# Kernel optimization log

Measured on AMD Instinct MI355X. Metric: run time of the kernel, lower is better.

Reference implementation:

```python
import jax, jax.numpy as jnp
import numpy as np

N, C, H, W = 10, 512, 40, 40
HW = H * W
OUT_CH = 128
EPS = 1e-12

def _l2norm(x, axis):
    # matches F.normalize: v / max(||v||_2, eps)
    n = jnp.sqrt(jnp.sum(x * x, axis=axis, keepdims=True))
    return x / jnp.maximum(n, EPS)

def _conv(x, w, b, pad):
    y = jax.lax.conv_general_dilated(
        x, w, window_strides=(1, 1), padding=[(pad, pad), (pad, pad)],
        dimension_numbers=('NCHW', 'OIHW', 'NCHW'))
    return y + b[None, :, None, None]

def setup_inputs() -> dict:
    key = jax.random.key(0)
    ks = jax.random.split(key, 6)
    feats = jax.random.normal(ks[0], (N, C, H, W), jnp.float32)
    SISMs = jax.random.uniform(ks[1], (N, 1, H, W), jnp.float32)
    # ResNetBlock(HW -> 128) params (Kaiming-uniform-ish fan-in bounds)
    s1 = float(1.0 / np.sqrt(HW * 9))
    s2 = float(1.0 / np.sqrt(OUT_CH * 9))
    ss = float(1.0 / np.sqrt(HW))
    w1 = jax.random.uniform(ks[2], (OUT_CH, HW, 3, 3), jnp.float32, -s1, s1)
    b1 = jnp.zeros((OUT_CH,), jnp.float32)
    w2 = jax.random.uniform(ks[3], (OUT_CH, OUT_CH, 3, 3), jnp.float32, -s2, s2)
    b2 = jnp.zeros((OUT_CH,), jnp.float32)
    ws = jax.random.uniform(ks[4], (OUT_CH, HW, 1, 1), jnp.float32, -ss, ss)
    bs = jnp.zeros((OUT_CH,), jnp.float32)
    return dict(feats=feats, SISMs=SISMs, w1=w1, b1=b1, w2=w2, b2=b2, ws=ws, bs=bs)

def reference(feats, SISMs, w1, b1, w2, b2, ws, bs):
    # SISMs supplied at (H,W): bilinear resize w/ align_corners=True at same size is identity
    NFs = _l2norm(feats, axis=1)                                   # (N,C,H,W)
    SIVs = _l2norm(jnp.mean(NFs * SISMs, axis=(-1, -2)), axis=1)   # (N,C)
    # CFM: 1x1 conv of NFs with SIVs as filters -> (N,N,H,W)
    cm = jnp.einsum('nchw,mc->nmhw', NFs, SIVs).reshape(N, N, HW)
    cm = _l2norm(cm, axis=2)
    corr = jnp.einsum('nmk,npk->nmp', cm, cm)                      # (N,N,N)
    wv = jax.nn.softmax(jnp.sum(corr, axis=2), axis=1)             # (N,N)
    CSA = jnp.sum(cm * wv[:, :, None], axis=1)                     # (N,HW)
    mn = jnp.min(CSA, axis=1, keepdims=True)
    mx = jnp.max(CSA, axis=1, keepdims=True)
    CSA = (CSA - mn) / (mx - mn + EPS)
    CSA_maps = CSA.reshape(N, 1, H, W)
    # self-correlation features: (N, HW, H, W)
    NFf = NFs.reshape(N, C, HW)
    SCFs = jnp.einsum('nci,ncj->nij', NFf, NFf).reshape(N, HW, H, W)
    # reorder channels by descending CSA evidence
    idx = jnp.argsort(-CSA, axis=1)                                # (N,HW)
    RSCFs = jnp.take_along_axis(SCFs, idx[:, :, None, None], axis=1)
    x = RSCFs * CSA_maps
    # ResNetBlock: relu(conv2(relu(conv1(x))) + shortcut_1x1(x))
    h = jax.nn.relu(_conv(x, w1, b1, 1))
    h = _conv(h, w2, b2, 1)
    sc = _conv(x, ws, bs, 0)
    return jax.nn.relu(h + sc)
```

## Files before the change

kernel.cpp:

```cpp
#include <hip/hip_runtime.h>
#include <hip/hip_bf16.h>
#include <math.h>

typedef short short8 __attribute__((ext_vector_type(8)));
typedef short short4v __attribute__((ext_vector_type(4)));
typedef float f32x4 __attribute__((ext_vector_type(4)));
typedef __hip_bfloat16 bf16;

#define KN 10
#define KC 512
#define KHW 1600
#define KH 40
#define KOC 128
#define KPW 42
#define KM 1280

__device__ __forceinline__ void gload16(const void* g, void* l) {
  __builtin_amdgcn_global_load_lds(
      (const __attribute__((address_space(1))) unsigned int*)g,
      (__attribute__((address_space(3))) unsigned int*)l, 16, 0, 0);
}

__device__ __forceinline__ double blockReduceSumD(double v) {
  __shared__ double tmpS[8];
  int lane = threadIdx.x & 63, wv = threadIdx.x >> 6;
  #pragma unroll
  for (int o = 32; o > 0; o >>= 1) v += __shfl_down(v, o);
  if (lane == 0) tmpS[wv] = v;
  __syncthreads();
  if (threadIdx.x == 0) {
    int nw = (blockDim.x + 63) >> 6;
    double s = 0;
    for (int i = 0; i < nw; i++) s += tmpS[i];
    tmpS[0] = s;
  }
  __syncthreads();
  double r = tmpS[0];
  __syncthreads();
  return r;
}

__device__ __forceinline__ double blockReduceMinD(double v) {
  __shared__ double tmpMn[8];
  int lane = threadIdx.x & 63, wv = threadIdx.x >> 6;
  #pragma unroll
  for (int o = 32; o > 0; o >>= 1) v = fmin(v, __shfl_down(v, o));
  if (lane == 0) tmpMn[wv] = v;
  __syncthreads();
  if (threadIdx.x == 0) {
    int nw = (blockDim.x + 63) >> 6;
    double s = tmpMn[0];
    for (int i = 1; i < nw; i++) s = fmin(s, tmpMn[i]);
    tmpMn[0] = s;
  }
  __syncthreads();
  double r = tmpMn[0];
  __syncthreads();
  return r;
}

__device__ __forceinline__ double blockReduceMaxD(double v) {
  __shared__ double tmpMx[8];
  int lane = threadIdx.x & 63, wv = threadIdx.x >> 6;
  #pragma unroll
  for (int o = 32; o > 0; o >>= 1) v = fmax(v, __shfl_down(v, o));
  if (lane == 0) tmpMx[wv] = v;
  __syncthreads();
  if (threadIdx.x == 0) {
    int nw = (blockDim.x + 63) >> 6;
    double s = tmpMx[0];
    for (int i = 1; i < nw; i++) s = fmax(s, tmpMx[i]);
    tmpMx[0] = s;
  }
  __syncthreads();
  double r = tmpMx[0];
  __syncthreads();
  return r;
}


__global__ void k_rnormp(const float* __restrict__ feats, double* __restrict__ ps) {
  int t = blockIdx.x * 256 + threadIdx.x;
  if (t >= KN * KHW) return;
  int ci = blockIdx.y;
  int n = t / KHW, k = t % KHW;
  const float* p = feats + (size_t)n * KC * KHW + (size_t)ci * 32 * KHW + k;
  double s = 0.0;
  #pragma unroll
  for (int c = 0; c < 32; ++c) { double v = p[(size_t)c * KHW]; s += v * v; }
  ps[(size_t)ci * KN * KHW + t] = s;
}

__global__ void k_rnormc(const double* __restrict__ ps, double* __restrict__ rnorm) {
  int t = blockIdx.x * 256 + threadIdx.x;
  if (t >= KN * KHW) return;
  double s = 0;
  #pragma unroll
  for (int ci = 0; ci < 16; ci++) s += ps[(size_t)ci * KN * KHW + t];
  double nn = sqrt(s);
  if (nn < 1e-12) nn = 1e-12;
  rnorm[t] = 1.0 / nn;
}

__global__ void k_nft(const float* __restrict__ feats, const double* __restrict__ rnorm,
                      const float* __restrict__ sism, bf16* __restrict__ NFT,
                      double* __restrict__ vpp) {
  __shared__ float T[32][33];
  int n = blockIdx.z, k0 = blockIdx.x * 32, c0 = blockIdx.y * 32;
  int tx = threadIdx.x, ty = threadIdx.y;
  const float* fb = feats + ((size_t)n * KC + c0) * KHW + k0;
  #pragma unroll
  for (int ii = 0; ii < 4; ii++) {
    int cl = ty * 4 + ii;
    T[cl][tx] = fb[(size_t)cl * KHW + tx];
  }
  __syncthreads();
  bf16* ob = NFT + ((size_t)n * KHW + k0) * KC + c0;
  #pragma unroll
  for (int ii = 0; ii < 4; ii++) {
    int kl = ty * 4 + ii;
    float r = (float)rnorm[n * KHW + k0 + kl];
    ob[(size_t)kl * KC + tx] = __float2bfloat16(T[tx][kl] * r);
  }
  double rs = rnorm[n * KHW + k0 + tx] * (double)sism[n * KHW + k0 + tx];
  #pragma unroll
  for (int ii = 0; ii < 4; ii++) {
    int cl = ty * 4 + ii;
    double v = (double)T[cl][tx] * rs;
    #pragma unroll
    for (int o = 16; o > 0; o >>= 1) v += __shfl_down(v, o, 32);
    if (tx == 0) vpp[((size_t)n * KC + c0 + cl) * 50 + k0 / 32] = v;
  }
}

__global__ void k_sivnorm2(const double* __restrict__ vpp, double* __restrict__ SIV) {
  int n = blockIdx.x, c = threadIdx.x;
  const double* p = vpp + ((size_t)n * KC + c) * 50;
  double acc = 0;
  #pragma unroll 5
  for (int j = 0; j < 50; j++) acc += p[j];
  acc /= (double)KHW;
  double s2 = blockReduceSumD(acc * acc);
  double nn = sqrt(s2);
  if (nn < 1e-12) nn = 1e-12;
  SIV[n * KC + c] = acc / nn;
}

__global__ void k_cmP(const float* __restrict__ feats, const double* __restrict__ SIV,
                      double* __restrict__ cmp) {
  __shared__ double sv[KN][32];
  int kc = blockIdx.x, ci = blockIdx.y, n = blockIdx.z;
  for (int t = threadIdx.x; t < KN * 32; t += 256) {
    int m = t / 32, c = t % 32;
    sv[m][c] = SIV[m * KC + ci * 32 + c];
  }
  __syncthreads();
  int k = kc * 256 + threadIdx.x;
  if (k >= KHW) return;
  const float* f = feats + ((size_t)n * KC + ci * 32) * KHW + k;
  double acc[KN];
  #pragma unroll
  for (int m = 0; m < KN; m++) acc[m] = 0.0;
  for (int c = 0; c < 32; ++c) {
    double fv = f[(size_t)c * KHW];
    #pragma unroll
    for (int m = 0; m < KN; m++) acc[m] += fv * sv[m][c];
  }
  const size_t str = (size_t)KN * KN * KHW;
  #pragma unroll
  for (int m = 0; m < KN; m++)
    cmp[(size_t)ci * str + ((size_t)n * KN + m) * KHW + k] = acc[m];
}

__global__ void k_cmBN(const double* __restrict__ cmp, const double* __restrict__ rnorm,
                       double* __restrict__ cm) {
  int b = blockIdx.x;
  int n = b / KN;
  const size_t str = (size_t)KN * KN * KHW;
  const size_t rb = (size_t)b * KHW;
  double v[4];
  int cnt = 0;
  double ss = 0;
  for (int k = threadIdx.x; k < KHW; k += 512) {
    double s = 0;
    #pragma unroll
    for (int ci = 0; ci < 16; ci++) s += cmp[ci * str + rb + k];
    s *= rnorm[n * KHW + k];
    v[cnt++] = s;
    ss += s * s;
  }
  ss = blockReduceSumD(ss);
  double nn = sqrt(ss);
  if (nn < 1e-12) nn = 1e-12;
  double rn = 1.0 / nn;
  cnt = 0;
  for (int k = threadIdx.x; k < KHW; k += 512) cm[rb + k] = v[cnt++] * rn;
}

__global__ void k_st(const double* __restrict__ cm, double* __restrict__ tbuf) {
  int b = blockIdx.x;
  int n = b / KN, m = b % KN;
  const double* base = cm + (size_t)n * KN * KHW;
  double acc = 0;
  for (int k = threadIdx.x; k < KHW; k += 256) {
    double S = 0;
    #pragma unroll
    for (int mm = 0; mm < KN; mm++) S += base[(size_t)mm * KHW + k];
    acc += base[(size_t)m * KHW + k] * S;
  }
  acc = blockReduceSumD(acc);
  if (threadIdx.x == 0) tbuf[b] = acc;
}

__global__ void k_csa(const double* __restrict__ cm, const double* __restrict__ tbuf,
                      double* __restrict__ CSAd, float* __restrict__ CSAf) {
  __shared__ double w[KN];
  int n = blockIdx.x, tid = threadIdx.x;
  if (tid == 0) {
    double v[KN], mx = -1e300;
    #pragma unroll
    for (int m = 0; m < KN; m++) { v[m] = tbuf[n * KN + m]; mx = fmax(mx, v[m]); }
    double s = 0;
    #pragma unroll
    for (int m = 0; m < KN; m++) { v[m] = exp(v[m] - mx); s += v[m]; }
    #pragma unroll
    for (int m = 0; m < KN; m++) w[m] = v[m] / s;
  }
  __syncthreads();
  double v[7];
  int cnt = 0;
  double lmin = 1e300, lmax = -1e300;
  for (int k = tid; k < KHW; k += 256) {
    double a = 0;
    #pragma unroll
    for (int m = 0; m < KN; m++) a += cm[((size_t)n * KN + m) * KHW + k] * w[m];
    v[cnt++] = a;
    lmin = fmin(lmin, a);
    lmax = fmax(lmax, a);
  }
  double mn = blockReduceMinD(lmin);
  double mx = blockReduceMaxD(lmax);
  double inv = 1.0 / (mx - mn + 1e-12);
  cnt = 0;
  for (int k = tid; k < KHW; k += 256) {
    double nv = (v[cnt++] - mn) * inv;
    CSAd[(size_t)n * KHW + k] = nv;
    CSAf[(size_t)n * KHW + k] = (float)nv;
  }
}

__global__ void k_rank(const double* __restrict__ CSAd, int* __restrict__ idx) {
  __shared__ double key[KHW];
  int b = blockIdx.x;
  int n = b / 100, it = b % 100;
  const double* src = CSAd + (size_t)n * KHW;
  for (int j = threadIdx.x; j < KHW; j += 256) key[j] = src[j];
  __syncthreads();
  int wave = threadIdx.x >> 6, lane = threadIdx.x & 63;
  int i0 = it * 16 + wave * 4;
  double ki[4];
  #pragma unroll
  for (int ii = 0; ii < 4; ii++) ki[ii] = key[i0 + ii];
  int r[4] = {0, 0, 0, 0};
  #pragma unroll
  for (int q = 0; q < 25; q++) {
    int j = q * 64 + lane;
    double kj = key[j];
    #pragma unroll
    for (int ii = 0; ii < 4; ii++) {
      int i = i0 + ii;
      r[ii] += (kj > ki[ii]) || (kj == ki[ii] && j < i);
    }
  }
  #pragma unroll
  for (int ii = 0; ii < 4; ii++) {
    int v = r[ii];
    #pragma unroll
    for (int o = 32; o > 0; o >>= 1) v += __shfl_down(v, o);
    if (lane == 0) idx[n * KHW + v] = i0 + ii;
  }
}

__global__ void k_prepw1s(const float* __restrict__ w1, const float* __restrict__ wsc,
                          bf16* __restrict__ w1s) {
  int t = blockIdx.x * 256 + threadIdx.x;
  int m = t / KHW, i = t % KHW;
  int tau = m >> 7, o = m & 127;
  float v = (tau < 9) ? w1[((size_t)o * KHW + i) * 9 + tau]
                      : wsc[(size_t)o * KHW + i];
  w1s[t] = __float2bfloat16(v);
}

__global__ void k_prepw2(const float* __restrict__ w2, bf16* __restrict__ w2p) {
  int t = blockIdx.x * 256 + threadIdx.x;
  if (t >= KOC * 9 * KOC) return;
  int o = t / (9 * KOC), r = t % (9 * KOC);
  int s = r / KOC, i = r % KOC;
  w2p[t] = __float2bfloat16(w2[(size_t)o * 9 * KOC + (size_t)i * 9 + s]);
}

__global__ void k_zborder(bf16* __restrict__ Zpad, bf16* __restrict__ hpadT) {
  int t = blockIdx.x * 256 + threadIdx.x;
  const int ZW = KN * 164 * (KC / 8);
  const int HWm = KN * 164 * (KOC / 8);
  int b;
  if (t < ZW) {
    int n = t / (164 * 64), r = t % (164 * 64);
    b = r / 64;
    int c8 = r % 64;
    int y, x;
    if (b < 42) { y = 0; x = b; }
    else if (b < 84) { y = 41; x = b - 42; }
    else if (b < 124) { y = b - 84 + 1; x = 0; }
    else { y = b - 124 + 1; x = 41; }
    short8 z = {};
    *(short8*)((short*)Zpad + ((size_t)n * KPW * KPW + (size_t)y * KPW + x) * KC + c8 * 8) = z;
  } else if (t < ZW + HWm) {
    int u = t - ZW;
    int n = u / (164 * 16), r = u % (164 * 16);
    b = r / 16;
    int c8 = r % 16;
    int y, x;
    if (b < 42) { y = 0; x = b; }
    else if (b < 84) { y = 41; x = b - 42; }
    else if (b < 124) { y = b - 84 + 1; x = 0; }
    else { y = b - 124 + 1; x = 41; }
    short8 z = {};
    *(short8*)((short*)hpadT + ((size_t)n * KPW * KPW + (size_t)y * KPW + x) * KOC + c8 * 8) = z;
  }
}

__global__ void k_gath2(const short* __restrict__ NFT, const int* __restrict__ idx,
                        short* __restrict__ NFcg) {
  __shared__ short T[32][33];
  int i0 = blockIdx.x * 32, c0 = blockIdx.y * 32, n = blockIdx.z;
  int tx = threadIdx.x, ty = threadIdx.y;
  #pragma unroll
  for (int ii = 0; ii < 4; ii++) {
    int row = ty * 4 + ii;
    int id = idx[n * KHW + i0 + row];
    T[row][tx] = NFT[((size_t)n * KHW + id) * KC + c0 + tx];
  }
  __syncthreads();
  #pragma unroll
  for (int ii = 0; ii < 4; ii++) {
    int cl = ty * 4 + ii;
    NFcg[((size_t)n * KC + c0 + cl) * KHW + i0 + tx] = T[tx][cl];
  }
}

__global__ void k_zprep(const bf16* __restrict__ NFT, const float* __restrict__ CSAf,
                        bf16* __restrict__ Zpad) {
  int t = blockIdx.x * 256 + threadIdx.x;
  const int per_n = KHW * (KC / 4);
  int n = t / per_n, r = t % per_n;
  int p = r / (KC / 4), cq = r % (KC / 4);
  float cs = CSAf[n * KHW + p];
  const short* src = (const short*)(NFT + ((size_t)n * KHW + p) * KC) + cq * 4;
  short4v v = *(const short4v*)src;
  short4v o;
  #pragma unroll
  for (int j = 0; j < 4; j++) {
    short s = v[j];
    bf16 hb = *reinterpret_cast<bf16*>(&s);
    bf16 res = __float2bfloat16(__bfloat162float(hb) * cs);
    o[j] = *reinterpret_cast<short*>(&res);
  }
  int y = p / KH, x = p % KH;
  short* dst = (short*)(Zpad + ((size_t)n * KPW * KPW + (size_t)(y + 1) * KPW + (x + 1)) * KC) + cq * 4;
  *(short4v*)dst = o;
}

__global__ __launch_bounds__(256) void k_gemmU(const short* __restrict__ w1s,
                                               const short* __restrict__ NFcg,
                                               bf16* __restrict__ Uc,
                                               bf16* __restrict__ Usc) {
  __shared__ __align__(16) short smem[24576];
  short* As = smem;
  short* Bs = smem + 8192;
  short* Cs = smem;
  int b = blockIdx.x;
  int workid = (b & 7) * 100 + (b >> 3);
  int pair = workid / 20;
  int th = workid % 20;
  int n = pair >> 2, c0 = (pair & 3) * 128;
  int tau = th >> 1, half = th & 1;
  int m0 = tau * 128 + half * 64;
  int tid = threadIdx.x, lane = tid & 63, wave = tid >> 6;
  int quad = lane >> 4, l15 = lane & 15;
  int wm = (wave & 1) * 32, wn = (wave >> 1) * 64;
  int sk = ((tid & 7) ^ ((tid >> 3) & 7)) * 8;
  int rowg = tid >> 3;
  const short* Bb = NFcg + (size_t)n * KC * KHW;
  const short* pA[2];
  #pragma unroll
  for (int g = 0; g < 2; g++)
    pA[g] = w1s + (size_t)(m0 + g * 32 + rowg) * KHW + sk;
  const short* pB[4];
  #pragma unroll
  for (int g = 0; g < 4; g++)
    pB[g] = Bb + (size_t)(c0 + g * 32 + rowg) * KHW + sk;
  char* lA = (char*)As + tid * 16;
  char* lB = (char*)Bs + tid * 16;
  int bq = (l15 >> 2) & 1;
  int qx = (quad ^ (l15 & 3)) * 8;
  int koff0 = 32 * bq + qx;
  int koff1 = 32 * (1 - bq) + qx;
  f32x4 acc[2][4] = {};
  gload16(pA[0], lA); gload16(pA[1], lA + 4096);
  gload16(pB[0], lB); gload16(pB[1], lB + 4096);
  gload16(pB[2], lB + 8192); gload16(pB[3], lB + 12288);
  __syncthreads();
  const int NS = 25;
  for (int s = 0; s < NS; s++) {
    int cb = s & 1, nb = cb ^ 1;
    if (s + 1 < NS) {
      int off = (s + 1) * 64;
      char* la = lA + nb * 8192;
      char* lb = lB + nb * 16384;
      gload16(pA[0] + off, la); gload16(pA[1] + off, la + 4096);
      gload16(pB[0] + off, lb); gload16(pB[1] + off, lb + 4096);
      gload16(pB[2] + off, lb + 8192); gload16(pB[3] + off, lb + 12288);
    }
    const short* Ab = As + cb * 4096;
    const short* Bbf = Bs + cb * 8192;
    #pragma unroll
    for (int ks = 0; ks < 2; ks++) {
      int ko = (ks == 0) ? koff0 : koff1;
      short8 av[2], bv[4];
      #pragma unroll
      for (int t = 0; t < 2; t++) av[t] = *(const short8*)&Ab[(wm + t * 16 + l15) * 64 + ko];
      #pragma unroll
      for (int t = 0; t < 4; t++) bv[t] = *(const short8*)&Bbf[(wn + t * 16 + l15) * 64 + ko];
      #pragma unroll
      for (int ti = 0; ti < 2; ti++)
        #pragma unroll
        for (int tj = 0; tj < 4; tj++)
          acc[ti][tj] = __builtin_amdgcn_mfma_f32_16x16x32_bf16(av[ti], bv[tj], acc[ti][tj], 0, 0, 0);
    }
    __syncthreads();
  }
  #pragma unroll
  for (int ti = 0; ti < 2; ti++) {
    int lr = wm + ti * 16 + quad * 4;
    #pragma unroll
    for (int tj = 0; tj < 4; tj++) {
      int lc = wn + tj * 16 + l15;
      #pragma unroll
      for (int r = 0; r < 4; r++)
        *(bf16*)&Cs[(lr + r) * 136 + lc] = __float2bfloat16(acc[ti][tj][r]);
    }
  }
  __syncthreads();
  int dyq = tau / 3, dxq = tau % 3;
  #pragma unroll
  for (int pass = 0; pass < 4; pass++) {
    int row = pass * 16 + (tid >> 4);
    int col = (tid & 15) * 8;
    if (tau < 9) {
      *(float4*)&Uc[((size_t)((n * 3 + dyq) * 128 + half * 64 + row)) * 1536 + dxq * 512 + c0 + col] =
          *(const float4*)&Cs[row * 136 + col];
    } else {
      *(float4*)&Usc[((size_t)(n * 128 + half * 64 + row)) * 512 + c0 + col] =
          *(const float4*)&Cs[row * 136 + col];
    }
  }
}

__global__ __launch_bounds__(256) void k_convh(const short* __restrict__ Uc,
                                               const short* __restrict__ Usc,
                                               const short* __restrict__ Zpad,
                                               float* __restrict__ Hpart) {
  __shared__ __align__(16) short smem[24576];
  short* As = smem;
  short* Bs = smem + 16384;
  int b = blockIdx.x;
  bool isconv = (b < 750);
  int n, dy, pt;
  if (isconv) {
    int xcd = b & 7, bi = b >> 3;
    int wgid = (xcd < 6 ? xcd * 94 : 6 * 94 + (xcd - 6) * 93) + bi;
    n = wgid / 75;
    int rest = wgid % 75;
    dy = rest / 25; pt = rest % 25;
  } else {
    int u = b - 750;
    n = u / 25; pt = u % 25; dy = 3;
  }
  int p0 = pt * 64;
  int tid = threadIdx.x, lane = tid & 63, wave = tid >> 6;
  int quad = lane >> 4, l15 = lane & 15;
  int wm = (wave & 1) * 64, wn = (wave >> 1) * 32;
  int sk = ((tid & 7) ^ ((tid >> 3) & 7)) * 8;
  int rowg = tid >> 3;
  const short* Zb = Zpad + (size_t)n * KPW * KPW * KC;
  const short* Abase = isconv ? Uc + ((size_t)((n * 3 + dy) * 128)) * 1536
                              : Usc + ((size_t)(n * 128)) * 512;
  int astr = isconv ? 1536 : 512;
  const short* pA[4];
  #pragma unroll
  for (int g = 0; g < 4; g++)
    pA[g] = Abase + (size_t)(g * 32 + rowg) * astr + sk;
  const short* pB[2];
  #pragma unroll
  for (int g = 0; g < 2; g++) {
    int p = p0 + g * 32 + rowg;
    int y = p / KH, x = p % KH;
    int yy = isconv ? (y + dy) : (y + 1);
    int xx = isconv ? x : (x + 1);
    pB[g] = Zb + ((size_t)yy * KPW + xx) * KC + sk;
  }
  char* lA = (char*)As + tid * 16;
  char* lB = (char*)Bs + tid * 16;
  int NS = isconv ? 24 : 8;
  int bq = (l15 >> 2) & 1;
  int qx = (quad ^ (l15 & 3)) * 8;
  int koff0 = 32 * bq + qx;
  int koff1 = 32 * (1 - bq) + qx;
  f32x4 acc[4][2] = {};
  gload16(pA[0], lA); gload16(pA[1], lA + 4096);
  gload16(pA[2], lA + 8192); gload16(pA[3], lA + 12288);
  gload16(pB[0], lB); gload16(pB[1], lB + 4096);
  __syncthreads();
  for (int s = 0; s < NS; s++) {
    int cb = s & 1, nb = cb ^ 1;
    if (s + 1 < NS) {
      int off = (s + 1) * 64;
      char* la = lA + nb * 16384;
      char* lb = lB + nb * 8192;
      gload16(pA[0] + off, la); gload16(pA[1] + off, la + 4096);
      gload16(pA[2] + off, la + 8192); gload16(pA[3] + off, la + 12288);
      gload16(pB[0] + off, lb); gload16(pB[1] + off, lb + 4096);
    }
    const short* Ab = As + cb * 8192;
    const short* Bb = Bs + cb * 4096;
    #pragma unroll
    for (int ks = 0; ks < 2; ks++) {
      int ko = (ks == 0) ? koff0 : koff1;
      short8 av[4], bv[2];
      #pragma unroll
      for (int t = 0; t < 4; t++) av[t] = *(const short8*)&Ab[(wm + t * 16 + l15) * 64 + ko];
      #pragma unroll
      for (int t = 0; t < 2; t++) bv[t] = *(const short8*)&Bb[(wn + t * 16 + l15) * 64 + ko];
      #pragma unroll
      for (int ti = 0; ti < 4; ti++)
        #pragma unroll
        for (int tj = 0; tj < 2; tj++)
          acc[ti][tj] = __builtin_amdgcn_mfma_f32_16x16x32_bf16(av[ti], bv[tj], acc[ti][tj], 0, 0, 0);
    }
    __syncthreads();
  }
  float* cbp = Hpart + ((size_t)(dy * KN + n)) * KOC * KHW;
  #pragma unroll
  for (int ti = 0; ti < 4; ti++) {
    int o = wm + ti * 16 + quad * 4;
    #pragma unroll
    for (int tj = 0; tj < 2; tj++) {
      int q = p0 + wn + tj * 16 + l15;
      #pragma unroll
      for (int r = 0; r < 4; r++)
        cbp[(size_t)(o + r) * KHW + q] = acc[ti][tj][r];
    }
  }
}

__global__ void k_hprep3(const float* __restrict__ Hpart, const float* __restrict__ b1,
                         bf16* __restrict__ hpadT) {
  __shared__ float T[32][132];
  int n = blockIdx.y, p0 = blockIdx.x * 32;
  int tx = threadIdx.x, ty = threadIdx.y;
  const size_t str = (size_t)KN * KOC * KHW;
  const float* hb = Hpart + (size_t)n * KOC * KHW;
  #pragma unroll
  for (int oc = 0; oc < 16; oc++) {
    int o = oc * 8 + ty;
    size_t off = (size_t)o * KHW + p0 + tx;
    T[tx][o] = fmaxf(hb[off] + hb[str + off] + hb[2 * str + off] + b1[o], 0.0f);
  }
  __syncthreads();
  bf16* hp = hpadT + (size_t)n * KPW * KPW * KOC;
  #pragma unroll
  for (int pc = 0; pc < 4; pc++) {
    int pl = ty * 4 + pc;
    int pp = p0 + pl;
    int yy = pp / KH, xx = pp % KH;
    bf16* row = hp + ((size_t)(yy + 1) * KPW + (xx + 1)) * KOC;
    #pragma unroll
    for (int u = 0; u < 4; u++) row[tx * 4 + u] = __float2bfloat16(T[pl][tx * 4 + u]);
  }
}

__global__ __launch_bounds__(256) void k_conv2f(const short* __restrict__ w2p,
                                                const short* __restrict__ hpadT,
                                                const float* __restrict__ Hpart,
                                                const float* __restrict__ b2,
                                                const float* __restrict__ bs,
                                                float* __restrict__ out) {
  __shared__ __align__(16) short smem[20480];
  short* As = smem;
  short* Bs = smem + 16384;
  int b = blockIdx.x;
  int xcd = b & 7, bi = b >> 3;
  int wgid = (xcd < 4 ? xcd * 63 : 4 * 63 + (xcd - 4) * 62) + bi;
  int n = wgid / 50, pt = wgid % 50;
  int p0 = pt * 32;
  int tid = threadIdx.x, lane = tid & 63, wave = tid >> 6;
  int quad = lane >> 4, l15 = lane & 15;
  int wm = (wave & 1) * 64, wn = (wave >> 1) * 16;
  int sk = ((tid & 7) ^ ((tid >> 3) & 7)) * 8;
  int rowg = tid >> 3;
  const short* hb = hpadT + (size_t)n * KPW * KPW * KOC;
  const short* pA[4];
  #pragma unroll
  for (int g = 0; g < 4; g++)
    pA[g] = w2p + (size_t)(g * 32 + rowg) * (9 * KOC) + sk;
  int prow = p0 + rowg;
  int py = prow / KH, px = prow % KH;
  const short* pB0 = hb + ((size_t)py * KPW + px) * KOC + sk;
  char* lA = (char*)As + tid * 16;
  char* lB = (char*)Bs + tid * 16;
  int bq = (l15 >> 2) & 1;
  int qx = (quad ^ (l15 & 3)) * 8;
  int koff0 = 32 * bq + qx;
  int koff1 = 32 * (1 - bq) + qx;
  f32x4 acc[4] = {};
  const int NS = 18;
  gload16(pA[0], lA); gload16(pA[1], lA + 4096);
  gload16(pA[2], lA + 8192); gload16(pA[3], lA + 12288);
  gload16(pB0, lB);
  __syncthreads();
  for (int s = 0; s < NS; s++) {
    int cb = s & 1, nb = cb ^ 1;
    if (s + 1 < NS) {
      int s2 = s + 1;
      int dy = s2 / 6, dxq = (s2 % 6) >> 1, kh = (s2 & 1) * 64;
      int ao = (dy * 3 + dxq) * 128 + kh;
      int bo = (dy * 42 + dxq) * 128 + kh;
      char* la = lA + nb * 16384;
      char* lb = lB + nb * 4096;
      gload16(pA[0] + ao, la); gload16(pA[1] + ao, la + 4096);
      gload16(pA[2] + ao, la + 8192); gload16(pA[3] + ao, la + 12288);
      gload16(pB0 + bo, lb);
    }
    const short* Ab = As + cb * 8192;
    const short* Bb = Bs + cb * 2048;
    #pragma unroll
    for (int ks = 0; ks < 2; ks++) {
      int ko = (ks == 0) ? koff0 : koff1;
      short8 av[4], bv;
      #pragma unroll
      for (int t = 0; t < 4; t++) av[t] = *(const short8*)&Ab[(wm + t * 16 + l15) * 64 + ko];
      bv = *(const short8*)&Bb[(wn + l15) * 64 + ko];
      #pragma unroll
      for (int ti = 0; ti < 4; ti++)
        acc[ti] = __builtin_amdgcn_mfma_f32_16x16x32_bf16(av[ti], bv, acc[ti], 0, 0, 0);
    }
    __syncthreads();
  }
  const float* hsc = Hpart + ((size_t)(3 * KN + n)) * KOC * KHW;
  float* ob = out + (size_t)n * KOC * KHW;
  int q = p0 + wn + l15;
  #pragma unroll
  for (int ti = 0; ti < 4; ti++) {
    int o = wm + ti * 16 + quad * 4;
    f32x4 b2v = *(const f32x4*)&b2[o];
    f32x4 bsv = *(const f32x4*)&bs[o];
    #pragma unroll
    for (int r = 0; r < 4; r++) {
      float v = acc[ti][r] + b2v[r] + bsv[r] + hsc[(size_t)(o + r) * KHW + q];
      ob[(size_t)(o + r) * KHW + q] = fmaxf(v, 0.0f);
    }
  }
}

extern "C" void kernel_launch(void* const* d_in, const int* in_sizes, int n_in,
                              void* d_out, int out_size, void* d_ws, size_t ws_size,
                              hipStream_t stream) {
  const float* feats = (const float*)d_in[0];
  const float* sisms = (const float*)d_in[1];
  const float* w1 = (const float*)d_in[2];
  const float* b1 = (const float*)d_in[3];
  const float* w2 = (const float*)d_in[4];
  const float* b2 = (const float*)d_in[5];
  const float* wsc = (const float*)d_in[6];
  const float* bsc = (const float*)d_in[7];
  float* out = (float*)d_out;

  char* w = (char*)d_ws;
  auto carve = [&](size_t bytes) -> void* {
    void* p = (void*)w;
    w += (bytes + 255) & ~(size_t)255;
    return p;
  };
  bf16* NFT   = (bf16*)carve((size_t)KN * KHW * KC * 2);
  bf16* NFcg  = (bf16*)carve((size_t)KN * KC * KHW * 2);
  bf16* Uc    = (bf16*)carve((size_t)KN * 3 * 128 * 1536 * 2);
  bf16* Usc   = (bf16*)carve((size_t)KN * 128 * 512 * 2);
  bf16* w1s   = (bf16*)carve((size_t)KM * KHW * 2);
  bf16* Zpad  = (bf16*)carve((size_t)KN * KPW * KPW * KC * 2);
  bf16* hpadT = (bf16*)carve((size_t)KN * KPW * KPW * KOC * 2);
  float* Hpart = (float*)carve((size_t)4 * KN * KOC * KHW * 4);
  bf16* w2p   = (bf16*)carve((size_t)KOC * 9 * KOC * 2);
  double* psbuf = (double*)carve((size_t)16 * KN * KHW * 8);
  double* rnorm = (double*)carve((size_t)KN * KHW * 8);
  double* vpp   = (double*)carve((size_t)KN * KC * 50 * 8);
  double* SIV   = (double*)carve((size_t)KN * KC * 8);
  double* cmp   = (double*)carve((size_t)16 * KN * KN * KHW * 8);
  double* cm    = (double*)carve((size_t)KN * KN * KHW * 8);
  double* tbuf  = (double*)carve((size_t)KN * KN * 8);
  double* CSAd  = (double*)carve((size_t)KN * KHW * 8);
  float* CSAf   = (float*)carve((size_t)KN * KHW * 4);
  int* idxb     = (int*)carve((size_t)KN * KHW * 4);

  k_zborder<<<513, 256, 0, stream>>>(Zpad, hpadT);

  k_rnormp<<<dim3(63, 16), 256, 0, stream>>>(feats, psbuf);
  k_rnormc<<<63, 256, 0, stream>>>(psbuf, rnorm);
  k_nft<<<dim3(50, 16, KN), dim3(32, 8), 0, stream>>>(feats, rnorm, sisms, NFT, vpp);
  k_sivnorm2<<<KN, 512, 0, stream>>>(vpp, SIV);
  k_cmP<<<dim3(7, 16, KN), 256, 0, stream>>>(feats, SIV, cmp);
  k_cmBN<<<KN * KN, 512, 0, stream>>>(cmp, rnorm, cm);
  k_st<<<KN * KN, 256, 0, stream>>>(cm, tbuf);
  k_csa<<<KN, 256, 0, stream>>>(cm, tbuf, CSAd, CSAf);
  k_rank<<<1000, 256, 0, stream>>>(CSAd, idxb);

  k_prepw1s<<<KM * KHW / 256, 256, 0, stream>>>(w1, wsc, w1s);
  k_prepw2<<<576, 256, 0, stream>>>(w2, w2p);
  k_gath2<<<dim3(50, 16, KN), dim3(32, 8), 0, stream>>>((const short*)NFT, idxb, (short*)NFcg);
  k_zprep<<<KN * KHW * (KC / 4) / 256, 256, 0, stream>>>(NFT, CSAf, Zpad);

  k_gemmU<<<800, 256, 0, stream>>>((const short*)w1s, (const short*)NFcg, Uc, Usc);
  k_convh<<<1000, 256, 0, stream>>>((const short*)Uc, (const short*)Usc,
                                    (const short*)Zpad, Hpart);
  k_hprep3<<<dim3(50, KN), dim3(32, 8), 0, stream>>>(Hpart, b1, hpadT);
  k_conv2f<<<500, 256, 0, stream>>>((const short*)w2p, (const short*)hpadT,
                                    Hpart, b2, bsc, out);
}
```

Measured before the change: 270.6 us.

## Merge prep kernels into fewer launches and vectorize feature loads

The weight conversion and border-zeroing kernels become one launch, k_prep, dispatched by block index, and the gather-transpose and Zpad fill become one launch, k_gz. k_rnormp and the smem fill in k_nft now read float4 instead of scalars, and k_rnormp launches fewer blocks with four accumulators per thread. The aim is to cut launch overhead and the gaps between small kernels, and to issue wider global loads. In exchange, the branch-dispatched kernels are heterogeneous, and the k_gz gather path runs __syncthreads inside a branch that is uniform per block.

```diff
diff --git a/kernel.cpp b/kernel.cpp
--- a/kernel.cpp
+++ b/kernel.cpp
@@ -80,15 +80,23 @@
 
 
 __global__ void k_rnormp(const float* __restrict__ feats, double* __restrict__ ps) {
-  int t = blockIdx.x * 256 + threadIdx.x;
-  if (t >= KN * KHW) return;
+  int t4 = blockIdx.x * 256 + threadIdx.x;
+  if (t4 >= KN * KHW / 4) return;
   int ci = blockIdx.y;
-  int n = t / KHW, k = t % KHW;
+  int k4 = t4 * 4;
+  int n = k4 / KHW, k = k4 % KHW;
   const float* p = feats + (size_t)n * KC * KHW + (size_t)ci * 32 * KHW + k;
-  double s = 0.0;
-  #pragma unroll
-  for (int c = 0; c < 32; ++c) { double v = p[(size_t)c * KHW]; s += v * v; }
-  ps[(size_t)ci * KN * KHW + t] = s;
+  double s0 = 0, s1 = 0, s2 = 0, s3 = 0;
+  #pragma unroll
+  for (int c = 0; c < 32; ++c) {
+    float4 v = *(const float4*)&p[(size_t)c * KHW];
+    s0 += (double)v.x * v.x;
+    s1 += (double)v.y * v.y;
+    s2 += (double)v.z * v.z;
+    s3 += (double)v.w * v.w;
+  }
+  double* pd = ps + (size_t)ci * KN * KHW + (size_t)n * KHW + k;
+  pd[0] = s0; pd[1] = s1; pd[2] = s2; pd[3] = s3;
 }
 
 __global__ void k_rnormc(const double* __restrict__ ps, double* __restrict__ rnorm) {
@@ -109,10 +117,13 @@
   int n = blockIdx.z, k0 = blockIdx.x * 32, c0 = blockIdx.y * 32;
   int tx = threadIdx.x, ty = threadIdx.y;
   const float* fb = feats + ((size_t)n * KC + c0) * KHW + k0;
-  #pragma unroll
-  for (int ii = 0; ii < 4; ii++) {
-    int cl = ty * 4 + ii;
-    T[cl][tx] = fb[(size_t)cl * KHW + tx];
+  {
+    int tid = ty * 32 + tx;
+    int cc = tid >> 3;
+    int k4 = (tid & 7) * 4;
+    float4 v = *(const float4*)&fb[(size_t)cc * KHW + k4];
+    T[cc][k4 + 0] = v.x; T[cc][k4 + 1] = v.y;
+    T[cc][k4 + 2] = v.z; T[cc][k4 + 3] = v.w;
   }
   __syncthreads();
   bf16* ob = NFT + ((size_t)n * KHW + k0) * KC + c0;
@@ -281,94 +292,97 @@
   }
 }
 
-__global__ void k_prepw1s(const float* __restrict__ w1, const float* __restrict__ wsc,
-                          bf16* __restrict__ w1s) {
-  int t = blockIdx.x * 256 + threadIdx.x;
-  int m = t / KHW, i = t % KHW;
-  int tau = m >> 7, o = m & 127;
-  float v = (tau < 9) ? w1[((size_t)o * KHW + i) * 9 + tau]
-                      : wsc[(size_t)o * KHW + i];
-  w1s[t] = __float2bfloat16(v);
-}
-
-__global__ void k_prepw2(const float* __restrict__ w2, bf16* __restrict__ w2p) {
-  int t = blockIdx.x * 256 + threadIdx.x;
-  if (t >= KOC * 9 * KOC) return;
-  int o = t / (9 * KOC), r = t % (9 * KOC);
-  int s = r / KOC, i = r % KOC;
-  w2p[t] = __float2bfloat16(w2[(size_t)o * 9 * KOC + (size_t)i * 9 + s]);
-}
-
-__global__ void k_zborder(bf16* __restrict__ Zpad, bf16* __restrict__ hpadT) {
-  int t = blockIdx.x * 256 + threadIdx.x;
-  const int ZW = KN * 164 * (KC / 8);
-  const int HWm = KN * 164 * (KOC / 8);
-  int b;
-  if (t < ZW) {
-    int n = t / (164 * 64), r = t % (164 * 64);
-    b = r / 64;
-    int c8 = r % 64;
-    int y, x;
-    if (b < 42) { y = 0; x = b; }
-    else if (b < 84) { y = 41; x = b - 42; }
-    else if (b < 124) { y = b - 84 + 1; x = 0; }
-    else { y = b - 124 + 1; x = 41; }
-    short8 z = {};
-    *(short8*)((short*)Zpad + ((size_t)n * KPW * KPW + (size_t)y * KPW + x) * KC + c8 * 8) = z;
-  } else if (t < ZW + HWm) {
-    int u = t - ZW;
-    int n = u / (164 * 16), r = u % (164 * 16);
-    b = r / 16;
-    int c8 = r % 16;
-    int y, x;
-    if (b < 42) { y = 0; x = b; }
-    else if (b < 84) { y = 41; x = b - 42; }
-    else if (b < 124) { y = b - 84 + 1; x = 0; }
-    else { y = b - 124 + 1; x = 41; }
-    short8 z = {};
-    *(short8*)((short*)hpadT + ((size_t)n * KPW * KPW + (size_t)y * KPW + x) * KOC + c8 * 8) = z;
-  }
-}
-
-__global__ void k_gath2(const short* __restrict__ NFT, const int* __restrict__ idx,
-                        short* __restrict__ NFcg) {
+__global__ void k_prep(const float* __restrict__ w1, const float* __restrict__ wsc,
+                       const float* __restrict__ w2,
+                       bf16* __restrict__ w1s, bf16* __restrict__ w2p,
+                       bf16* __restrict__ Zpad, bf16* __restrict__ hpadT) {
+  int b = blockIdx.x;
+  if (b < 8000) {
+    int t = b * 256 + threadIdx.x;
+    int m = t / KHW, i = t % KHW;
+    int tau = m >> 7, o = m & 127;
+    float v = (tau < 9) ? w1[((size_t)o * KHW + i) * 9 + tau]
+                        : wsc[(size_t)o * KHW + i];
+    w1s[t] = __float2bfloat16(v);
+  } else if (b < 8576) {
+    int t = (b - 8000) * 256 + threadIdx.x;
+    if (t >= KOC * 9 * KOC) return;
+    int o = t / (9 * KOC), r = t % (9 * KOC);
+    int s = r / KOC, i = r % KOC;
+    w2p[t] = __float2bfloat16(w2[(size_t)o * 9 * KOC + (size_t)i * 9 + s]);
+  } else {
+    int t = (b - 8576) * 256 + threadIdx.x;
+    const int ZW = KN * 164 * (KC / 8);
+    const int HWm = KN * 164 * (KOC / 8);
+    int bb;
+    if (t < ZW) {
+      int n = t / (164 * 64), r = t % (164 * 64);
+      bb = r / 64;
+      int c8 = r % 64;
+      int y, x;
+      if (bb < 42) { y = 0; x = bb; }
+      else if (bb < 84) { y = 41; x = bb - 42; }
+      else if (bb < 124) { y = bb - 84 + 1; x = 0; }
+      else { y = bb - 124 + 1; x = 41; }
+      short8 z = {};
+      *(short8*)((short*)Zpad + ((size_t)n * KPW * KPW + (size_t)y * KPW + x) * KC + c8 * 8) = z;
+    } else if (t < ZW + HWm) {
+      int u = t - ZW;
+      int n = u / (164 * 16), r = u % (164 * 16);
+      bb = r / 16;
+      int c8 = r % 16;
+      int y, x;
+      if (bb < 42) { y = 0; x = bb; }
+      else if (bb < 84) { y = 41; x = bb - 42; }
+      else if (bb < 124) { y = bb - 84 + 1; x = 0; }
+      else { y = bb - 124 + 1; x = 41; }
+      short8 z = {};
+      *(short8*)((short*)hpadT + ((size_t)n * KPW * KPW + (size_t)y * KPW + x) * KOC + c8 * 8) = z;
+    }
+  }
+}
+
+__global__ void k_gz(const short* __restrict__ NFT, const int* __restrict__ idx,
+                     const float* __restrict__ CSAf,
+                     short* __restrict__ NFcg, bf16* __restrict__ Zpad) {
   __shared__ short T[32][33];
-  int i0 = blockIdx.x * 32, c0 = blockIdx.y * 32, n = blockIdx.z;
+  int b = blockIdx.x;
   int tx = threadIdx.x, ty = threadIdx.y;
-  #pragma unroll
-  for (int ii = 0; ii < 4; ii++) {
-    int row = ty * 4 + ii;
-    int id = idx[n * KHW + i0 + row];
-    T[row][tx] = NFT[((size_t)n * KHW + id) * KC + c0 + tx];
-  }
-  __syncthreads();
-  #pragma unroll
-  for (int ii = 0; ii < 4; ii++) {
-    int cl = ty * 4 + ii;
-    NFcg[((size_t)n * KC + c0 + cl) * KHW + i0 + tx] = T[tx][cl];
-  }
-}
-
-__global__ void k_zprep(const bf16* __restrict__ NFT, const float* __restrict__ CSAf,
-                        bf16* __restrict__ Zpad) {
-  int t = blockIdx.x * 256 + threadIdx.x;
-  const int per_n = KHW * (KC / 4);
-  int n = t / per_n, r = t % per_n;
-  int p = r / (KC / 4), cq = r % (KC / 4);
-  float cs = CSAf[n * KHW + p];
-  const short* src = (const short*)(NFT + ((size_t)n * KHW + p) * KC) + cq * 4;
-  short4v v = *(const short4v*)src;
-  short4v o;
-  #pragma unroll
-  for (int j = 0; j < 4; j++) {
-    short s = v[j];
-    bf16 hb = *reinterpret_cast<bf16*>(&s);
-    bf16 res = __float2bfloat16(__bfloat162float(hb) * cs);
-    o[j] = *reinterpret_cast<short*>(&res);
-  }
-  int y = p / KH, x = p % KH;
-  short* dst = (short*)(Zpad + ((size_t)n * KPW * KPW + (size_t)(y + 1) * KPW + (x + 1)) * KC) + cq * 4;
-  *(short4v*)dst = o;
+  if (b < 8000) {
+    int n = b / 800, r = b % 800;
+    int c0 = (r / 50) * 32, i0 = (r % 50) * 32;
+    #pragma unroll
+    for (int ii = 0; ii < 4; ii++) {
+      int row = ty * 4 + ii;
+      int id = idx[n * KHW + i0 + row];
+      T[row][tx] = NFT[((size_t)n * KHW + id) * KC + c0 + tx];
+    }
+    __syncthreads();
+    #pragma unroll
+    for (int ii = 0; ii < 4; ii++) {
+      int cl = ty * 4 + ii;
+      NFcg[((size_t)n * KC + c0 + cl) * KHW + i0 + tx] = T[tx][cl];
+    }
+  } else {
+    int t = (b - 8000) * 256 + (ty * 32 + tx);
+    const int per_n = KHW * (KC / 4);
+    int n = t / per_n, r = t % per_n;
+    int p = r / (KC / 4), cq = r % (KC / 4);
+    float cs = CSAf[n * KHW + p];
+    const short* src = (const short*)(NFT + ((size_t)n * KHW + p) * KC) + cq * 4;
+    short4v v = *(const short4v*)src;
+    short4v o;
+    #pragma unroll
+    for (int j = 0; j < 4; j++) {
+      short s = v[j];
+      bf16 hb = *reinterpret_cast<bf16*>(&s);
+      bf16 res = __float2bfloat16(__bfloat162float(hb) * cs);
+      o[j] = *reinterpret_cast<short*>(&res);
+    }
+    int y = p / KH, x = p % KH;
+    short* dst = (short*)(Zpad + ((size_t)n * KPW * KPW + (size_t)(y + 1) * KPW + (x + 1)) * KC) + cq * 4;
+    *(short4v*)dst = o;
+  }
 }
 
 __global__ __launch_bounds__(256) void k_gemmU(const short* __restrict__ w1s,
@@ -712,9 +726,9 @@
   float* CSAf   = (float*)carve((size_t)KN * KHW * 4);
   int* idxb     = (int*)carve((size_t)KN * KHW * 4);
 
-  k_zborder<<<513, 256, 0, stream>>>(Zpad, hpadT);
-
-  k_rnormp<<<dim3(63, 16), 256, 0, stream>>>(feats, psbuf);
+  k_prep<<<9089, 256, 0, stream>>>(w1, wsc, w2, w1s, w2p, Zpad, hpadT);
+
+  k_rnormp<<<dim3(16, 16), 256, 0, stream>>>(feats, psbuf);
   k_rnormc<<<63, 256, 0, stream>>>(psbuf, rnorm);
   k_nft<<<dim3(50, 16, KN), dim3(32, 8), 0, stream>>>(feats, rnorm, sisms, NFT, vpp);
   k_sivnorm2<<<KN, 512, 0, stream>>>(vpp, SIV);
@@ -724,10 +738,8 @@
   k_csa<<<KN, 256, 0, stream>>>(cm, tbuf, CSAd, CSAf);
   k_rank<<<1000, 256, 0, stream>>>(CSAd, idxb);
 
-  k_prepw1s<<<KM * KHW / 256, 256, 0, stream>>>(w1, wsc, w1s);
-  k_prepw2<<<576, 256, 0, stream>>>(w2, w2p);
-  k_gath2<<<dim3(50, 16, KN), dim3(32, 8), 0, stream>>>((const short*)NFT, idxb, (short*)NFcg);
-  k_zprep<<<KN * KHW * (KC / 4) / 256, 256, 0, stream>>>(NFT, CSAf, Zpad);
+  k_gz<<<16000, dim3(32, 8), 0, stream>>>((const short*)NFT, idxb, CSAf,
+                                          (short*)NFcg, Zpad);
 
   k_gemmU<<<800, 256, 0, stream>>>((const short*)w1s, (const short*)NFcg, Uc, Usc);
   k_convh<<<1000, 256, 0, stream>>>((const short*)Uc, (const short*)Usc,
```

Measured after the change: 262.2 us. -3.1%, faster.
